# Kernel optimization log

Measured on AMD Instinct MI355X. Metric: run time of the kernel, lower is better.

## Reference

```python
import jax, jax.numpy as jnp
import numpy as np

B, N, F, FOBS, D = 4, 1024, 128, 32, 128
K_HOP = 3  # os.environ k_hop default 3


def setup_inputs() -> dict:
    key = jax.random.key(0)
    k0, k1, k2, k3, k4 = jax.random.split(key, 5)
    X = jax.random.normal(k0, (B, N, F), jnp.float32)
    # xavier-ish scales for params
    a_link = jax.random.normal(k1, (FOBS, 1), jnp.float32) * (1.414 / np.sqrt(FOBS + 1))
    W0 = jax.random.normal(k2, (F, D), jnp.float32) * np.sqrt(2.0 / (F + D))
    W1 = jax.random.normal(k3, (D, D), jnp.float32) * np.sqrt(1.0 / D)
    W2 = jax.random.normal(k4, (D, D), jnp.float32) * np.sqrt(1.0 / D)
    return {"X": X, "a_link": a_link, "W0": W0, "W1": W1, "W2": W2}


def reference(X, a_link, W0, W1, W2):
    eye = jnp.eye(N, dtype=X.dtype)

    def per_graph(Xb):  # Xb: [N, F]
        h = Xb[:, :FOBS]                                   # [N, FOBS]
        # e_ij = a_link^T |h_i - h_j|
        e = jnp.einsum('ijf,fo->ij', jnp.abs(h[:, None, :] - h[None, :, :]), a_link)
        A = jax.nn.sigmoid(e)
        A = A * (1.0 - eye)                                # zero diagonal (A - diag(diag(A)))
        Dm = jnp.zeros_like(A)                             # diag(diag(A)) is zero after removal
        A_hat = A + eye
        d_inv_sqrt = jnp.sum(A_hat, axis=1) ** -0.5        # row sums (dim=1 in mini_batch path)
        norm = d_inv_sqrt[:, None] * A_hat * d_inv_sqrt[None, :]  # D^-1/2 A_hat D^-1/2
        H = norm @ (Xb @ W0)                               # k = 0
        for Wk in (W1, W2):                                # k = 1 .. K_HOP-1 (norm detached in torch)
            H = jax.lax.stop_gradient(norm) @ (H @ Wk)
        return jax.nn.relu(H), A, Dm

    Hs, As, Ds = jax.vmap(per_graph)(X)
    return Hs, As, X, Ds
```

## Files before the change

kernel.cpp:

```cpp
#include <hip/hip_runtime.h>
#include <math.h>

#define BB 4
#define NN 1024
#define FF 128
#define DD 128
#define FOBS 32

typedef __attribute__((ext_vector_type(8))) short bfrag;
typedef __attribute__((ext_vector_type(4))) float ffrag;
typedef __attribute__((ext_vector_type(4))) unsigned short us4;

__device__ __forceinline__ unsigned short f2bf(float x) {
    unsigned u = __builtin_bit_cast(unsigned, x);
    u += 0x7fffu + ((u >> 16) & 1u);
    return (unsigned short)(u >> 16);
}
__device__ __forceinline__ float bf2f(unsigned short s) {
    unsigned u = (unsigned)s << 16;
    return __builtin_bit_cast(float, u);
}
__device__ __forceinline__ void gload16(const void* g, void* l) {
    __builtin_amdgcn_global_load_lds((const __attribute__((address_space(1))) unsigned*)g,
                                     (__attribute__((address_space(3))) unsigned*)l, 16, 0, 0);
}
__device__ __forceinline__ void compute_dinv16(const float* __restrict__ Pp, int b, int n0,
                                               int tid, float* dinv_s) {
    int r = tid >> 4, p = tid & 15;
    float s = Pp[((size_t)b * NN + n0 + r) * 16 + p];
    s += __shfl_xor(s, 1);
    s += __shfl_xor(s, 2);
    s += __shfl_xor(s, 4);
    s += __shfl_xor(s, 8);
    if (p == 0) dinv_s[r] = rsqrtf(1.f + s);
}

__global__ __launch_bounds__(256) void zero_f4(float4* __restrict__ p, int n4) {
    int i = blockIdx.x * 256 + threadIdx.x;
    if (i < n4) p[i] = make_float4(0.f, 0.f, 0.f, 0.f);
}

__global__ __launch_bounds__(256) void adj_kernel(const float* __restrict__ X,
                                                  const float* __restrict__ a_link,
                                                  const float* __restrict__ W0,
                                                  const float* __restrict__ W1,
                                                  const float* __restrict__ W2,
                                                  float* __restrict__ A,
                                                  unsigned short* __restrict__ Abf,
                                                  unsigned short* __restrict__ Xbf,
                                                  unsigned short* __restrict__ Wt,
                                                  float* __restrict__ Pp,
                                                  float* __restrict__ Xo,
                                                  float* __restrict__ Zd) {
    int tid = threadIdx.x;
    if (blockIdx.z == 5) {
        if (Zd) {
            int q = blockIdx.y * 16 + blockIdx.x;
            float4* Z = (float4*)Zd;
#pragma unroll
            for (int p = 0; p < 16; p++)
                Z[(size_t)q * 4096 + p * 256 + tid] = make_float4(0.f, 0.f, 0.f, 0.f);
        }
        return;
    }
    if (blockIdx.z == 4) {
        int q = (blockIdx.y * 16 + blockIdx.x) * 256 + tid;
        if (q < 49152) {
            int m = q >> 14, rem = q & 16383, fp = rem >> 7, f = rem & 127;
            const float* W = (m == 0) ? W0 : (m == 1) ? W1 : W2;
            Wt[q] = f2bf(W[(size_t)f * 128 + fp]);
        } else {
            int u = q - 49152;
#pragma unroll
            for (int p = 0; p < 8; p++) {
                size_t i4 = (size_t)u + (size_t)p * 16384;
                float4 v = *(const float4*)&X[i4 * 4];
                us4 o; o[0] = f2bf(v.x); o[1] = f2bf(v.y); o[2] = f2bf(v.z); o[3] = f2bf(v.w);
                *(us4*)&Xbf[i4 * 4] = o;
            }
        }
        return;
    }
    int b = blockIdx.z, i0 = blockIdx.y * 64, j0 = blockIdx.x * 64;
    __shared__ float hi[64][FOBS + 1];
    __shared__ float hj[64][FOBS + 1];
    __shared__ float av[FOBS];
    __shared__ float part_s[64][16];
    const float* Xb = X + (size_t)b * NN * FF;
    if (j0 == 0) {
#pragma unroll
        for (int p = 0; p < 8; p++) {
            int c = p * 256 + tid, r = c >> 5, qq = c & 31;
            *(float4*)&Xo[((size_t)b * NN + i0 + r) * FF + qq * 4] =
                *(const float4*)&Xb[(size_t)(i0 + r) * FF + qq * 4];
        }
    }
#pragma unroll
    for (int l = 0; l < 8; l++) {
        int idx = l * 256 + tid;
        int r = idx >> 5, f = idx & 31;
        hi[r][f] = Xb[(size_t)(i0 + r) * FF + f];
        hj[r][f] = Xb[(size_t)(j0 + r) * FF + f];
    }
    if (tid < FOBS) av[tid] = a_link[tid];
    __syncthreads();

    int ty = tid >> 4, tx = tid & 15;
    int ir = ty * 4, jc = tx * 4;
    float acc[4][4] = {};
#pragma unroll
    for (int f = 0; f < FOBS; f++) {
        float a = av[f];
        float x[4], y[4];
#pragma unroll
        for (int r = 0; r < 4; r++) x[r] = hi[ir + r][f];
#pragma unroll
        for (int c = 0; c < 4; c++) y[c] = hj[jc + c][f];
#pragma unroll
        for (int r = 0; r < 4; r++)
#pragma unroll
            for (int c = 0; c < 4; c++)
                acc[r][c] += fabsf(x[r] - y[c]) * a;
    }
    float* Ab = A + (size_t)b * NN * NN;
    unsigned short* Abb = Abf + (size_t)b * NN * NN;
#pragma unroll
    for (int r = 0; r < 4; r++) {
        int gi = i0 + ir + r;
        float vv[4];
        float rs = 0.f;
#pragma unroll
        for (int c = 0; c < 4; c++) {
            int gj = j0 + jc + c;
            float sg = 1.f / (1.f + __expf(-acc[r][c]));
            vv[c] = (gi == gj) ? 0.f : sg;
            rs += vv[c];
        }
        *(float4*)&Ab[(size_t)gi * NN + (j0 + jc)] = make_float4(vv[0], vv[1], vv[2], vv[3]);
        us4 o; o[0] = f2bf(vv[0]); o[1] = f2bf(vv[1]); o[2] = f2bf(vv[2]); o[3] = f2bf(vv[3]);
        *(us4*)&Abb[(size_t)gi * NN + (j0 + jc)] = o;
        part_s[ir + r][tx] = rs;
    }
    __syncthreads();
    if (tid < 64) {
        float s = 0.f;
#pragma unroll
        for (int k = 0; k < 16; k++) s += part_s[tid][k];
        Pp[((size_t)b * NN + i0 + tid) * 16 + blockIdx.x] = s;
    }
}

__global__ __launch_bounds__(256) void gw0_kernel(const unsigned short* __restrict__ Xbf,
                                                  const unsigned short* __restrict__ Wt0,
                                                  const float* __restrict__ Pp,
                                                  unsigned short* __restrict__ TtOut) {
    int b = blockIdx.y;
    int n0 = blockIdx.x * 16;
    __shared__ unsigned short Wt_s[128 * 128];
    __shared__ unsigned short H_s[16 * 128];
    __shared__ float dinv_s[16];
    int tid = threadIdx.x;
    compute_dinv16(Pp, b, n0, tid, dinv_s);
    const unsigned short* Hb = Xbf + (size_t)b * NN * DD;
#pragma unroll
    for (int p = 0; p < 8; p++) {
        int c = p * 256 + tid, row = c >> 4, kc = c & 15;
        gload16(Wt0 + (size_t)row * 128 + ((kc ^ (row & 7)) * 8), Wt_s + (size_t)c * 8);
    }
    {
        int c = tid, row = c >> 4, kc = c & 15;
        gload16(Hb + (size_t)(n0 + row) * 128 + ((kc ^ (row & 7)) * 8), H_s + (size_t)c * 8);
    }
    __syncthreads();

    int w = tid >> 6, l = tid & 63, lr = l & 15, lg = l >> 4;
    ffrag acc[2] = {};
#pragma unroll
    for (int ks = 0; ks < 4; ks++) {
        int k0 = ks * 32 + lg * 8;
        bfrag a[2], bb;
#pragma unroll
        for (int rb = 0; rb < 2; rb++) {
            int row = w * 32 + rb * 16 + lr;
            int byt = (row * 256 + k0 * 2) ^ ((row & 7) << 4);
            a[rb] = *(const bfrag*)((const char*)Wt_s + byt);
        }
        {
            int row = lr;
            int byt = (row * 256 + k0 * 2) ^ ((row & 7) << 4);
            bb = *(const bfrag*)((const char*)H_s + byt);
        }
#pragma unroll
        for (int rb = 0; rb < 2; rb++)
            acc[rb] = __builtin_amdgcn_mfma_f32_16x16x32_bf16(a[rb], bb, acc[rb], 0, 0, 0);
    }
    unsigned short* Ttb = TtOut + (size_t)b * DD * NN;
    int nl = lr;
    float dv = dinv_s[nl];
#pragma unroll
    for (int rb = 0; rb < 2; rb++)
#pragma unroll
        for (int r = 0; r < 4; r++) {
            int f = w * 32 + rb * 16 + lg * 4 + r;
            Ttb[(size_t)f * NN + n0 + nl] = f2bf(acc[rb][r] * dv);
        }
}

template <int MODE>
__global__ __launch_bounds__(256) void ga_kernel(const unsigned short* __restrict__ Abf,
                                                 const unsigned short* __restrict__ Tt,
                                                 const unsigned short* __restrict__ WtN,
                                                 const float* __restrict__ Pp,
                                                 unsigned short* __restrict__ TtN,
                                                 float* __restrict__ HsF) {
    int b = blockIdx.y, n0 = blockIdx.x * 16;
    __shared__ unsigned short T_s[3 * 128 * 64];
    __shared__ unsigned short A_s[3 * 16 * 64];
    __shared__ unsigned short W_s[MODE == 0 ? 128 * 128 : 64];
    __shared__ float dinv_s[16];
    int tid = threadIdx.x;
    const unsigned short* Ttb = Tt + (size_t)b * DD * NN;
    const unsigned short* Ab = Abf + (size_t)b * NN * NN;

    compute_dinv16(Pp, b, n0, tid, dinv_s);

    if (MODE == 0) {
#pragma unroll
        for (int p = 0; p < 8; p++) {
            int c = p * 256 + tid, row = c >> 4, kc = c & 15;
            gload16(WtN + (size_t)row * 128 + ((kc ^ (row & 7)) * 8), W_s + (size_t)c * 8);
        }
    }
    auto stageT = [&](int buf, int kt) {
#pragma unroll
        for (int p = 0; p < 4; p++) {
            int c = p * 256 + tid, row = c >> 3, kc = c & 7;
            gload16(Ttb + (size_t)row * NN + kt + ((kc ^ (row & 7)) * 8),
                    T_s + (size_t)buf * (128 * 64) + (size_t)c * 8);
        }
        int c = tid & 127, row = c >> 3, kc = c & 7;
        gload16(Ab + (size_t)(n0 + row) * NN + kt + ((kc ^ (row & 7)) * 8),
                A_s + (size_t)buf * (16 * 64) + (size_t)c * 8);
    };
    stageT(0, 0);
    stageT(1, 64);

    int w = tid >> 6, l = tid & 63, lr = l & 15, lg = l >> 4;
    ffrag acc[2] = {};
    int cur = 0, sb = 2;
    for (int t = 0; t < 16; t++) {
        if (t <= 13) stageT(sb, (t + 2) * 64);
        if (t < 14)       asm volatile("s_waitcnt vmcnt(10)" ::: "memory");
        else if (t == 14) asm volatile("s_waitcnt vmcnt(5)"  ::: "memory");
        else              asm volatile("s_waitcnt vmcnt(0)"  ::: "memory");
        __builtin_amdgcn_s_barrier();
        asm volatile("" ::: "memory");
        const unsigned short* Tc = T_s + (size_t)cur * (128 * 64);
        const unsigned short* Ac = A_s + (size_t)cur * (16 * 64);
#pragma unroll
        for (int ks = 0; ks < 2; ks++) {
            int k0 = ks * 32 + lg * 8;
            bfrag a[2], bb;
#pragma unroll
            for (int rb = 0; rb < 2; rb++) {
                int row = w * 32 + rb * 16 + lr;
                int byt = (row * 128 + k0 * 2) ^ ((row & 7) << 4);
                a[rb] = *(const bfrag*)((const char*)Tc + byt);
            }
            {
                int row = lr;
                int byt = (row * 128 + k0 * 2) ^ ((row & 7) << 4);
                bb = *(const bfrag*)((const char*)Ac + byt);
            }
#pragma unroll
            for (int rb = 0; rb < 2; rb++)
                acc[rb] = __builtin_amdgcn_mfma_f32_16x16x32_bf16(a[rb], bb, acc[rb], 0, 0, 0);
        }
        asm volatile("s_waitcnt lgkmcnt(0)" ::: "memory");
        __builtin_amdgcn_s_barrier();
        cur = (cur == 2) ? 0 : cur + 1;
        sb = (sb == 2) ? 0 : sb + 1;
    }

    int nl = lr;
    float dv = dinv_s[nl];
    if (MODE == 1) {
#pragma unroll
        for (int rb = 0; rb < 2; rb++) {
            int f0 = w * 32 + rb * 16 + lg * 4;
            float v[4];
#pragma unroll
            for (int r = 0; r < 4; r++) {
                float idv = bf2f(Ttb[(size_t)(f0 + r) * NN + n0 + nl]);
                v[r] = fmaxf((acc[rb][r] + idv) * dv, 0.f);
            }
            *(float4*)&HsF[((size_t)b * NN + n0 + nl) * DD + f0] = make_float4(v[0], v[1], v[2], v[3]);
        }
        return;
    }
    unsigned short* H_s = T_s;
#pragma unroll
    for (int rb = 0; rb < 2; rb++) {
        int f0 = w * 32 + rb * 16 + lg * 4;
        us4 o;
#pragma unroll
        for (int r = 0; r < 4; r++) {
            float idv = bf2f(Ttb[(size_t)(f0 + r) * NN + n0 + nl]);
            o[r] = f2bf((acc[rb][r] + idv) * dv);
        }
        int byt = (nl * 256 + f0 * 2) ^ ((nl & 7) << 4);
        *(us4*)((char*)H_s + byt) = o;
    }
    __syncthreads();
    ffrag acc2[2] = {};
#pragma unroll
    for (int ks = 0; ks < 4; ks++) {
        int k0 = ks * 32 + lg * 8;
        bfrag a2[2], b2;
#pragma unroll
        for (int rb = 0; rb < 2; rb++) {
            int row = w * 32 + rb * 16 + lr;
            int byt = (row * 256 + k0 * 2) ^ ((row & 7) << 4);
            a2[rb] = *(const bfrag*)((const char*)W_s + byt);
        }
        {
            int row = lr;
            int byt = (row * 256 + k0 * 2) ^ ((row & 7) << 4);
            b2 = *(const bfrag*)((const char*)H_s + byt);
        }
#pragma unroll
        for (int rb = 0; rb < 2; rb++)
            acc2[rb] = __builtin_amdgcn_mfma_f32_16x16x32_bf16(a2[rb], b2, acc2[rb], 0, 0, 0);
    }
    unsigned short* TtNb = TtN + (size_t)b * DD * NN;
#pragma unroll
    for (int rb = 0; rb < 2; rb++)
#pragma unroll
        for (int r = 0; r < 4; r++) {
            int f2 = w * 32 + rb * 16 + lg * 4 + r;
            TtNb[(size_t)f2 * NN + n0 + nl] = f2bf(acc2[rb][r] * dv);
        }
}

extern "C" void kernel_launch(void* const* d_in, const int* in_sizes, int n_in,
                              void* d_out, int out_size, void* d_ws, size_t ws_size,
                              hipStream_t stream) {
    const float* X      = (const float*)d_in[0];
    const float* a_link = (const float*)d_in[1];
    const float* W0     = (const float*)d_in[2];
    const float* W1     = (const float*)d_in[3];
    const float* W2     = (const float*)d_in[4];
    float* out = (float*)d_out;

    const size_t HND = (size_t)BB * NN * DD;
    const size_t HNN = (size_t)BB * NN * NN;
    float* Hs = out;
    float* As = out + HND;
    float* Xo = out + HND + HNN;
    float* Ds = out + 2 * HND + HNN;

    const size_t NEED = 11894784;
    bool usews = (ws_size >= NEED);
    char* scr = usews ? (char*)d_ws : (char*)Ds;

    unsigned short* Abf = (unsigned short*)(scr);
    unsigned short* Xbf = (unsigned short*)(scr + 8388608);
    unsigned short* TtA = (unsigned short*)(scr + 9437184);
    unsigned short* TtB = (unsigned short*)(scr + 10485760);
    unsigned short* Wt  = (unsigned short*)(scr + 11534336);
    float* Pp           = (float*)(scr + 11632640);

    adj_kernel<<<dim3(16, 16, usews ? 6 : 5), 256, 0, stream>>>(
        X, a_link, W0, W1, W2, As, Abf, Xbf, Wt, Pp, Xo, usews ? Ds : nullptr);

    gw0_kernel<<<dim3(64, BB), 256, 0, stream>>>(Xbf, Wt, Pp, TtA);
    ga_kernel<0><<<dim3(64, BB), 256, 0, stream>>>(Abf, TtA, Wt + 16384, Pp, TtB, nullptr);
    ga_kernel<0><<<dim3(64, BB), 256, 0, stream>>>(Abf, TtB, Wt + 32768, Pp, TtA, nullptr);
    ga_kernel<1><<<dim3(64, BB), 256, 0, stream>>>(Abf, TtA, nullptr, Pp, nullptr, Hs);

    if (!usews)
        zero_f4<<<dim3(4096), 256, 0, stream>>>((float4*)Ds, (int)(HNN / 4));
}
```

Measured before the change: 48.70 us.

## Fuse all stages into one persistent kernel with grid barriers and folded normalization

```diff
diff --git a/kernel.cpp b/kernel.cpp
--- a/kernel.cpp
+++ b/kernel.cpp
@@ -6,6 +6,7 @@
 #define FF 128
 #define DD 128
 #define FOBS 32
+#define NBLK 256
 
 typedef __attribute__((ext_vector_type(8))) short bfrag;
 typedef __attribute__((ext_vector_type(4))) float ffrag;
@@ -16,231 +17,40 @@
     u += 0x7fffu + ((u >> 16) & 1u);
     return (unsigned short)(u >> 16);
 }
-__device__ __forceinline__ float bf2f(unsigned short s) {
-    unsigned u = (unsigned)s << 16;
-    return __builtin_bit_cast(float, u);
-}
 __device__ __forceinline__ void gload16(const void* g, void* l) {
     __builtin_amdgcn_global_load_lds((const __attribute__((address_space(1))) unsigned*)g,
                                      (__attribute__((address_space(3))) unsigned*)l, 16, 0, 0);
 }
-__device__ __forceinline__ void compute_dinv16(const float* __restrict__ Pp, int b, int n0,
-                                               int tid, float* dinv_s) {
-    int r = tid >> 4, p = tid & 15;
-    float s = Pp[((size_t)b * NN + n0 + r) * 16 + p];
-    s += __shfl_xor(s, 1);
-    s += __shfl_xor(s, 2);
-    s += __shfl_xor(s, 4);
-    s += __shfl_xor(s, 8);
-    if (p == 0) dinv_s[r] = rsqrtf(1.f + s);
-}
-
-__global__ __launch_bounds__(256) void zero_f4(float4* __restrict__ p, int n4) {
-    int i = blockIdx.x * 256 + threadIdx.x;
-    if (i < n4) p[i] = make_float4(0.f, 0.f, 0.f, 0.f);
-}
-
-__global__ __launch_bounds__(256) void adj_kernel(const float* __restrict__ X,
-                                                  const float* __restrict__ a_link,
-                                                  const float* __restrict__ W0,
-                                                  const float* __restrict__ W1,
-                                                  const float* __restrict__ W2,
-                                                  float* __restrict__ A,
-                                                  unsigned short* __restrict__ Abf,
-                                                  unsigned short* __restrict__ Xbf,
-                                                  unsigned short* __restrict__ Wt,
-                                                  float* __restrict__ Pp,
-                                                  float* __restrict__ Xo,
-                                                  float* __restrict__ Zd) {
-    int tid = threadIdx.x;
-    if (blockIdx.z == 5) {
-        if (Zd) {
-            int q = blockIdx.y * 16 + blockIdx.x;
-            float4* Z = (float4*)Zd;
-#pragma unroll
-            for (int p = 0; p < 16; p++)
-                Z[(size_t)q * 4096 + p * 256 + tid] = make_float4(0.f, 0.f, 0.f, 0.f);
-        }
-        return;
-    }
-    if (blockIdx.z == 4) {
-        int q = (blockIdx.y * 16 + blockIdx.x) * 256 + tid;
-        if (q < 49152) {
-            int m = q >> 14, rem = q & 16383, fp = rem >> 7, f = rem & 127;
-            const float* W = (m == 0) ? W0 : (m == 1) ? W1 : W2;
-            Wt[q] = f2bf(W[(size_t)f * 128 + fp]);
-        } else {
-            int u = q - 49152;
-#pragma unroll
-            for (int p = 0; p < 8; p++) {
-                size_t i4 = (size_t)u + (size_t)p * 16384;
-                float4 v = *(const float4*)&X[i4 * 4];
-                us4 o; o[0] = f2bf(v.x); o[1] = f2bf(v.y); o[2] = f2bf(v.z); o[3] = f2bf(v.w);
-                *(us4*)&Xbf[i4 * 4] = o;
-            }
-        }
-        return;
-    }
-    int b = blockIdx.z, i0 = blockIdx.y * 64, j0 = blockIdx.x * 64;
-    __shared__ float hi[64][FOBS + 1];
-    __shared__ float hj[64][FOBS + 1];
-    __shared__ float av[FOBS];
-    __shared__ float part_s[64][16];
-    const float* Xb = X + (size_t)b * NN * FF;
-    if (j0 == 0) {
-#pragma unroll
-        for (int p = 0; p < 8; p++) {
-            int c = p * 256 + tid, r = c >> 5, qq = c & 31;
-            *(float4*)&Xo[((size_t)b * NN + i0 + r) * FF + qq * 4] =
-                *(const float4*)&Xb[(size_t)(i0 + r) * FF + qq * 4];
-        }
-    }
-#pragma unroll
-    for (int l = 0; l < 8; l++) {
-        int idx = l * 256 + tid;
-        int r = idx >> 5, f = idx & 31;
-        hi[r][f] = Xb[(size_t)(i0 + r) * FF + f];
-        hj[r][f] = Xb[(size_t)(j0 + r) * FF + f];
-    }
-    if (tid < FOBS) av[tid] = a_link[tid];
+__device__ __forceinline__ void gbar(unsigned* cnt) {
     __syncthreads();
-
-    int ty = tid >> 4, tx = tid & 15;
-    int ir = ty * 4, jc = tx * 4;
-    float acc[4][4] = {};
-#pragma unroll
-    for (int f = 0; f < FOBS; f++) {
-        float a = av[f];
-        float x[4], y[4];
-#pragma unroll
-        for (int r = 0; r < 4; r++) x[r] = hi[ir + r][f];
-#pragma unroll
-        for (int c = 0; c < 4; c++) y[c] = hj[jc + c][f];
-#pragma unroll
-        for (int r = 0; r < 4; r++)
-#pragma unroll
-            for (int c = 0; c < 4; c++)
-                acc[r][c] += fabsf(x[r] - y[c]) * a;
-    }
-    float* Ab = A + (size_t)b * NN * NN;
-    unsigned short* Abb = Abf + (size_t)b * NN * NN;
-#pragma unroll
-    for (int r = 0; r < 4; r++) {
-        int gi = i0 + ir + r;
-        float vv[4];
-        float rs = 0.f;
-#pragma unroll
-        for (int c = 0; c < 4; c++) {
-            int gj = j0 + jc + c;
-            float sg = 1.f / (1.f + __expf(-acc[r][c]));
-            vv[c] = (gi == gj) ? 0.f : sg;
-            rs += vv[c];
-        }
-        *(float4*)&Ab[(size_t)gi * NN + (j0 + jc)] = make_float4(vv[0], vv[1], vv[2], vv[3]);
-        us4 o; o[0] = f2bf(vv[0]); o[1] = f2bf(vv[1]); o[2] = f2bf(vv[2]); o[3] = f2bf(vv[3]);
-        *(us4*)&Abb[(size_t)gi * NN + (j0 + jc)] = o;
-        part_s[ir + r][tx] = rs;
+    if (threadIdx.x == 0) {
+        __threadfence();
+        __hip_atomic_fetch_add(cnt, 1u, __ATOMIC_RELAXED, __HIP_MEMORY_SCOPE_AGENT);
+        while (__hip_atomic_load(cnt, __ATOMIC_RELAXED, __HIP_MEMORY_SCOPE_AGENT) < NBLK)
+            __builtin_amdgcn_s_sleep(8);
+        __threadfence();
     }
     __syncthreads();
-    if (tid < 64) {
-        float s = 0.f;
-#pragma unroll
-        for (int k = 0; k < 16; k++) s += part_s[tid][k];
-        Pp[((size_t)b * NN + i0 + tid) * 16 + blockIdx.x] = s;
-    }
-}
-
-__global__ __launch_bounds__(256) void gw0_kernel(const unsigned short* __restrict__ Xbf,
-                                                  const unsigned short* __restrict__ Wt0,
-                                                  const float* __restrict__ Pp,
-                                                  unsigned short* __restrict__ TtOut) {
-    int b = blockIdx.y;
-    int n0 = blockIdx.x * 16;
-    __shared__ unsigned short Wt_s[128 * 128];
-    __shared__ unsigned short H_s[16 * 128];
-    __shared__ float dinv_s[16];
-    int tid = threadIdx.x;
-    compute_dinv16(Pp, b, n0, tid, dinv_s);
-    const unsigned short* Hb = Xbf + (size_t)b * NN * DD;
-#pragma unroll
-    for (int p = 0; p < 8; p++) {
-        int c = p * 256 + tid, row = c >> 4, kc = c & 15;
-        gload16(Wt0 + (size_t)row * 128 + ((kc ^ (row & 7)) * 8), Wt_s + (size_t)c * 8);
-    }
-    {
-        int c = tid, row = c >> 4, kc = c & 15;
-        gload16(Hb + (size_t)(n0 + row) * 128 + ((kc ^ (row & 7)) * 8), H_s + (size_t)c * 8);
-    }
-    __syncthreads();
-
-    int w = tid >> 6, l = tid & 63, lr = l & 15, lg = l >> 4;
-    ffrag acc[2] = {};
-#pragma unroll
-    for (int ks = 0; ks < 4; ks++) {
-        int k0 = ks * 32 + lg * 8;
-        bfrag a[2], bb;
-#pragma unroll
-        for (int rb = 0; rb < 2; rb++) {
-            int row = w * 32 + rb * 16 + lr;
-            int byt = (row * 256 + k0 * 2) ^ ((row & 7) << 4);
-            a[rb] = *(const bfrag*)((const char*)Wt_s + byt);
-        }
-        {
-            int row = lr;
-            int byt = (row * 256 + k0 * 2) ^ ((row & 7) << 4);
-            bb = *(const bfrag*)((const char*)H_s + byt);
-        }
-#pragma unroll
-        for (int rb = 0; rb < 2; rb++)
-            acc[rb] = __builtin_amdgcn_mfma_f32_16x16x32_bf16(a[rb], bb, acc[rb], 0, 0, 0);
-    }
-    unsigned short* Ttb = TtOut + (size_t)b * DD * NN;
-    int nl = lr;
-    float dv = dinv_s[nl];
-#pragma unroll
-    for (int rb = 0; rb < 2; rb++)
-#pragma unroll
-        for (int r = 0; r < 4; r++) {
-            int f = w * 32 + rb * 16 + lg * 4 + r;
-            Ttb[(size_t)f * NN + n0 + nl] = f2bf(acc[rb][r] * dv);
-        }
-}
-
-template <int MODE>
-__global__ __launch_bounds__(256) void ga_kernel(const unsigned short* __restrict__ Abf,
-                                                 const unsigned short* __restrict__ Tt,
-                                                 const unsigned short* __restrict__ WtN,
-                                                 const float* __restrict__ Pp,
-                                                 unsigned short* __restrict__ TtN,
-                                                 float* __restrict__ HsF) {
-    int b = blockIdx.y, n0 = blockIdx.x * 16;
-    __shared__ unsigned short T_s[3 * 128 * 64];
-    __shared__ unsigned short A_s[3 * 16 * 64];
-    __shared__ unsigned short W_s[MODE == 0 ? 128 * 128 : 64];
-    __shared__ float dinv_s[16];
-    int tid = threadIdx.x;
-    const unsigned short* Ttb = Tt + (size_t)b * DD * NN;
-    const unsigned short* Ab = Abf + (size_t)b * NN * NN;
-
-    compute_dinv16(Pp, b, n0, tid, dinv_s);
-
-    if (MODE == 0) {
-#pragma unroll
-        for (int p = 0; p < 8; p++) {
-            int c = p * 256 + tid, row = c >> 4, kc = c & 15;
-            gload16(WtN + (size_t)row * 128 + ((kc ^ (row & 7)) * 8), W_s + (size_t)c * 8);
-        }
-    }
+}
+
+template <int LAST>
+__device__ __forceinline__ void ga_phase(const unsigned short* __restrict__ Sb,
+                                         const unsigned short* __restrict__ Tin,
+                                         unsigned short* __restrict__ Tout,
+                                         float* __restrict__ HsB,
+                                         int n0, int tid, char* smem) {
+    unsigned short* T_s = (unsigned short*)smem;
+    unsigned short* S_s = (unsigned short*)(smem + 49152);
     auto stageT = [&](int buf, int kt) {
 #pragma unroll
         for (int p = 0; p < 4; p++) {
             int c = p * 256 + tid, row = c >> 3, kc = c & 7;
-            gload16(Ttb + (size_t)row * NN + kt + ((kc ^ (row & 7)) * 8),
+            gload16(Tin + (size_t)row * NN + kt + ((kc ^ (row & 7)) * 8),
                     T_s + (size_t)buf * (128 * 64) + (size_t)c * 8);
         }
         int c = tid & 127, row = c >> 3, kc = c & 7;
-        gload16(Ab + (size_t)(n0 + row) * NN + kt + ((kc ^ (row & 7)) * 8),
-                A_s + (size_t)buf * (16 * 64) + (size_t)c * 8);
+        gload16(Sb + (size_t)(n0 + row) * NN + kt + ((kc ^ (row & 7)) * 8),
+                S_s + (size_t)buf * (16 * 64) + (size_t)c * 8);
     };
     stageT(0, 0);
     stageT(1, 64);
@@ -256,7 +66,7 @@
         __builtin_amdgcn_s_barrier();
         asm volatile("" ::: "memory");
         const unsigned short* Tc = T_s + (size_t)cur * (128 * 64);
-        const unsigned short* Ac = A_s + (size_t)cur * (16 * 64);
+        const unsigned short* Sc = S_s + (size_t)cur * (16 * 64);
 #pragma unroll
         for (int ks = 0; ks < 2; ks++) {
             int k0 = ks * 32 + lg * 8;
@@ -270,7 +80,7 @@
             {
                 int row = lr;
                 int byt = (row * 128 + k0 * 2) ^ ((row & 7) << 4);
-                bb = *(const bfrag*)((const char*)Ac + byt);
+                bb = *(const bfrag*)((const char*)Sc + byt);
             }
 #pragma unroll
             for (int rb = 0; rb < 2; rb++)
@@ -281,65 +91,268 @@
         cur = (cur == 2) ? 0 : cur + 1;
         sb = (sb == 2) ? 0 : sb + 1;
     }
-
-    int nl = lr;
-    float dv = dinv_s[nl];
-    if (MODE == 1) {
+    if (LAST) {
 #pragma unroll
         for (int rb = 0; rb < 2; rb++) {
             int f0 = w * 32 + rb * 16 + lg * 4;
             float v[4];
 #pragma unroll
+            for (int r = 0; r < 4; r++) v[r] = fmaxf(acc[rb][r], 0.f);
+            *(float4*)&HsB[(size_t)(n0 + lr) * DD + f0] = make_float4(v[0], v[1], v[2], v[3]);
+        }
+    } else {
+#pragma unroll
+        for (int rb = 0; rb < 2; rb++)
+#pragma unroll
             for (int r = 0; r < 4; r++) {
-                float idv = bf2f(Ttb[(size_t)(f0 + r) * NN + n0 + nl]);
-                v[r] = fmaxf((acc[rb][r] + idv) * dv, 0.f);
-            }
-            *(float4*)&HsF[((size_t)b * NN + n0 + nl) * DD + f0] = make_float4(v[0], v[1], v[2], v[3]);
-        }
-        return;
-    }
-    unsigned short* H_s = T_s;
-#pragma unroll
-    for (int rb = 0; rb < 2; rb++) {
-        int f0 = w * 32 + rb * 16 + lg * 4;
-        us4 o;
-#pragma unroll
-        for (int r = 0; r < 4; r++) {
-            float idv = bf2f(Ttb[(size_t)(f0 + r) * NN + n0 + nl]);
-            o[r] = f2bf((acc[rb][r] + idv) * dv);
-        }
-        int byt = (nl * 256 + f0 * 2) ^ ((nl & 7) << 4);
-        *(us4*)((char*)H_s + byt) = o;
-    }
-    __syncthreads();
-    ffrag acc2[2] = {};
-#pragma unroll
-    for (int ks = 0; ks < 4; ks++) {
-        int k0 = ks * 32 + lg * 8;
-        bfrag a2[2], b2;
+                int f = w * 32 + rb * 16 + lg * 4 + r;
+                Tout[(size_t)f * NN + n0 + lr] = f2bf(acc[rb][r]);
+            }
+    }
+}
+
+__global__ __launch_bounds__(256, 1) void fused_kernel(
+    const float* __restrict__ X, const float* __restrict__ a_link,
+    const float* __restrict__ W0, const float* __restrict__ W1, const float* __restrict__ W2,
+    float* __restrict__ As, float* __restrict__ Xo, float* __restrict__ Hs,
+    float* __restrict__ Ds,
+    unsigned short* __restrict__ Sbf, unsigned short* __restrict__ Xbf,
+    unsigned short* __restrict__ TtX, unsigned short* __restrict__ TtY,
+    unsigned short* __restrict__ W01t, unsigned short* __restrict__ W2t,
+    float* __restrict__ Pp, unsigned* cnt, int usews)
+{
+    __shared__ __align__(16) char smem[77824];
+    int tid = threadIdx.x;
+    int bid = blockIdx.x;
+
+    {
+        float* hi   = (float*)smem;
+        float* hj   = (float*)(smem + 8448);
+        float* av   = (float*)(smem + 16896);
+        float* part = (float*)(smem + 17024);
+        if (tid < FOBS) av[tid] = a_link[tid];
+        for (int it = 0; it < 4; it++) {
+            int t = bid * 4 + it;
+            int bt = t >> 8, rem = t & 255;
+            int i0 = (rem >> 4) * 64, j0 = (rem & 15) * 64;
+            const float* Xb = X + (size_t)bt * NN * FF;
+            __syncthreads();
+            if (j0 == 0) {
+#pragma unroll
+                for (int p = 0; p < 8; p++) {
+                    int c = p * 256 + tid, r = c >> 5, qq = c & 31;
+                    *(float4*)&Xo[((size_t)bt * NN + i0 + r) * FF + qq * 4] =
+                        *(const float4*)&Xb[(size_t)(i0 + r) * FF + qq * 4];
+                }
+            }
+#pragma unroll
+            for (int lq = 0; lq < 8; lq++) {
+                int idx = lq * 256 + tid;
+                int r = idx >> 5, f = idx & 31;
+                hi[r * 33 + f] = Xb[(size_t)(i0 + r) * FF + f];
+                hj[r * 33 + f] = Xb[(size_t)(j0 + r) * FF + f];
+            }
+            __syncthreads();
+            int ty = tid >> 4, tx = tid & 15;
+            int ir = ty * 4, jc = tx * 4;
+            float acc[4][4] = {};
+#pragma unroll
+            for (int f = 0; f < FOBS; f++) {
+                float a = av[f];
+                float x[4], y[4];
+#pragma unroll
+                for (int r = 0; r < 4; r++) x[r] = hi[(ir + r) * 33 + f];
+#pragma unroll
+                for (int c = 0; c < 4; c++) y[c] = hj[(jc + c) * 33 + f];
+#pragma unroll
+                for (int r = 0; r < 4; r++)
+#pragma unroll
+                    for (int c = 0; c < 4; c++)
+                        acc[r][c] += fabsf(x[r] - y[c]) * a;
+            }
+            float* Ab = As + (size_t)bt * NN * NN;
+#pragma unroll
+            for (int r = 0; r < 4; r++) {
+                int gi = i0 + ir + r;
+                float vv[4]; float rs = 0.f;
+#pragma unroll
+                for (int c = 0; c < 4; c++) {
+                    int gj = j0 + jc + c;
+                    float sg = 1.f / (1.f + __expf(-acc[r][c]));
+                    vv[c] = (gi == gj) ? 0.f : sg;
+                    rs += vv[c];
+                }
+                *(float4*)&Ab[(size_t)gi * NN + (j0 + jc)] = make_float4(vv[0], vv[1], vv[2], vv[3]);
+                part[(ir + r) * 16 + tx] = rs;
+            }
+            __syncthreads();
+            if (tid < 64) {
+                float s = 0.f;
+#pragma unroll
+                for (int k = 0; k < 16; k++) s += part[tid * 16 + k];
+                Pp[((size_t)bt * NN + i0 + tid) * 16 + (rem & 15)] = s;
+            }
+        }
+        if (bid < 16) {
+#pragma unroll
+            for (int q = 0; q < 4; q++) {
+                int e = q * 256 + tid;
+                int g = bid * 8 + (e >> 7), f = e & 127;
+                float s = 0.f;
+                for (int h = 0; h < 128; h++) s += W0[f * 128 + h] * W1[h * 128 + g];
+                W01t[g * 128 + f] = f2bf(s);
+            }
+        } else if (bid < 32) {
+#pragma unroll
+            for (int q = 0; q < 4; q++) {
+                int e = (bid - 16) * 1024 + q * 256 + tid;
+                int f2 = e >> 7, g = e & 127;
+                W2t[e] = f2bf(W2[g * 128 + f2]);
+            }
+        } else if (bid < 96) {
+#pragma unroll
+            for (int q = 0; q < 8; q++) {
+                size_t i4 = (size_t)(bid - 32) * 2048 + q * 256 + tid;
+                float4 v = *(const float4*)&X[i4 * 4];
+                us4 o; o[0] = f2bf(v.x); o[1] = f2bf(v.y); o[2] = f2bf(v.z); o[3] = f2bf(v.w);
+                *(us4*)&Xbf[i4 * 4] = o;
+            }
+        }
+    }
+    gbar(cnt + 0);
+
+    int b = bid >> 6, n0 = (bid & 63) * 16;
+    {
+        float* dinvF         = (float*)smem;
+        unsigned short* W01s = (unsigned short*)(smem + 4096);
+        unsigned short* W2s  = (unsigned short*)(smem + 36864);
+        unsigned short* Xps  = (unsigned short*)(smem + 69632);
+        unsigned short* Ps   = (unsigned short*)(smem + 73728);
+        const unsigned short* Xb = Xbf + (size_t)b * NN * DD;
+#pragma unroll
+        for (int p = 0; p < 8; p++) {
+            int c = p * 256 + tid, row = c >> 4, kc = c & 15;
+            gload16(W01t + (size_t)row * 128 + ((kc ^ (row & 7)) * 8), W01s + (size_t)c * 8);
+        }
+#pragma unroll
+        for (int p = 0; p < 8; p++) {
+            int c = p * 256 + tid, row = c >> 4, kc = c & 15;
+            gload16(W2t + (size_t)row * 128 + ((kc ^ (row & 7)) * 8), W2s + (size_t)c * 8);
+        }
+        {
+            int c = tid, row = c >> 4, kc = c & 15;
+            gload16(Xb + (size_t)(n0 + row) * 128 + ((kc ^ (row & 7)) * 8), Xps + (size_t)c * 8);
+        }
+#pragma unroll
+        for (int rr = 0; rr < 4; rr++) {
+            int row = tid * 4 + rr;
+            const float* pp = Pp + ((size_t)b * NN + row) * 16;
+            float s = 0.f;
+#pragma unroll
+            for (int k2 = 0; k2 < 16; k2++) s += pp[k2];
+            dinvF[row] = rsqrtf(1.f + s);
+        }
+        __syncthreads();
+        {
+            int r = tid >> 4, cg = tid & 15;
+            int gi = n0 + r;
+            const float* Ar = As + ((size_t)b * NN + gi) * NN;
+            unsigned short* Sr = Sbf + ((size_t)b * NN + gi) * NN;
+            float di = dinvF[gi];
+#pragma unroll
+            for (int c4 = 0; c4 < 16; c4++) {
+                int col = cg * 4 + c4 * 64;
+                float4 a4 = *(const float4*)&Ar[col];
+                us4 o;
+                o[0] = f2bf(di * dinvF[col + 0] * (a4.x + ((col + 0) == gi ? 1.f : 0.f)));
+                o[1] = f2bf(di * dinvF[col + 1] * (a4.y + ((col + 1) == gi ? 1.f : 0.f)));
+                o[2] = f2bf(di * dinvF[col + 2] * (a4.z + ((col + 2) == gi ? 1.f : 0.f)));
+                o[3] = f2bf(di * dinvF[col + 3] * (a4.w + ((col + 3) == gi ? 1.f : 0.f)));
+                *(us4*)&Sr[col] = o;
+            }
+        }
+        if (usews) {
+            float4* Z = (float4*)Ds;
+#pragma unroll
+            for (int q = 0; q < 16; q++)
+                Z[(size_t)bid * 4096 + q * 256 + tid] = make_float4(0.f, 0.f, 0.f, 0.f);
+        }
+        int w = tid >> 6, l = tid & 63, lr = l & 15, lg = l >> 4;
+        ffrag pacc[2] = {};
+#pragma unroll
+        for (int ks = 0; ks < 4; ks++) {
+            int k0 = ks * 32 + lg * 8;
+            bfrag a[2], bb;
+#pragma unroll
+            for (int rb = 0; rb < 2; rb++) {
+                int row = w * 32 + rb * 16 + lr;
+                int byt = (row * 256 + k0 * 2) ^ ((row & 7) << 4);
+                a[rb] = *(const bfrag*)((const char*)W01s + byt);
+            }
+            {
+                int byt = (lr * 256 + k0 * 2) ^ ((lr & 7) << 4);
+                bb = *(const bfrag*)((const char*)Xps + byt);
+            }
+#pragma unroll
+            for (int rb = 0; rb < 2; rb++)
+                pacc[rb] = __builtin_amdgcn_mfma_f32_16x16x32_bf16(a[rb], bb, pacc[rb], 0, 0, 0);
+        }
 #pragma unroll
         for (int rb = 0; rb < 2; rb++) {
-            int row = w * 32 + rb * 16 + lr;
-            int byt = (row * 256 + k0 * 2) ^ ((row & 7) << 4);
-            a2[rb] = *(const bfrag*)((const char*)W_s + byt);
-        }
-        {
-            int row = lr;
-            int byt = (row * 256 + k0 * 2) ^ ((row & 7) << 4);
-            b2 = *(const bfrag*)((const char*)H_s + byt);
-        }
+            int g0 = w * 32 + rb * 16 + lg * 4;
+            us4 o;
+#pragma unroll
+            for (int r = 0; r < 4; r++) o[r] = f2bf(pacc[rb][r]);
+            int byt = (lr * 256 + g0 * 2) ^ ((lr & 7) << 4);
+            *(us4*)((char*)Ps + byt) = o;
+        }
+        __syncthreads();
+        ffrag tacc[2] = {};
+#pragma unroll
+        for (int ks = 0; ks < 4; ks++) {
+            int k0 = ks * 32 + lg * 8;
+            bfrag a2[2], b2;
+#pragma unroll
+            for (int rb = 0; rb < 2; rb++) {
+                int row = w * 32 + rb * 16 + lr;
+                int byt = (row * 256 + k0 * 2) ^ ((row & 7) << 4);
+                a2[rb] = *(const bfrag*)((const char*)W2s + byt);
+            }
+            {
+                int byt = (lr * 256 + k0 * 2) ^ ((lr & 7) << 4);
+                b2 = *(const bfrag*)((const char*)Ps + byt);
+            }
+#pragma unroll
+            for (int rb = 0; rb < 2; rb++)
+                tacc[rb] = __builtin_amdgcn_mfma_f32_16x16x32_bf16(a2[rb], b2, tacc[rb], 0, 0, 0);
+        }
+        unsigned short* Tb = TtX + (size_t)b * DD * NN;
 #pragma unroll
         for (int rb = 0; rb < 2; rb++)
-            acc2[rb] = __builtin_amdgcn_mfma_f32_16x16x32_bf16(a2[rb], b2, acc2[rb], 0, 0, 0);
-    }
-    unsigned short* TtNb = TtN + (size_t)b * DD * NN;
-#pragma unroll
-    for (int rb = 0; rb < 2; rb++)
-#pragma unroll
-        for (int r = 0; r < 4; r++) {
-            int f2 = w * 32 + rb * 16 + lg * 4 + r;
-            TtNb[(size_t)f2 * NN + n0 + nl] = f2bf(acc2[rb][r] * dv);
-        }
+#pragma unroll
+            for (int r = 0; r < 4; r++) {
+                int f2 = w * 32 + rb * 16 + lg * 4 + r;
+                Tb[(size_t)f2 * NN + n0 + lr] = f2bf(tacc[rb][r]);
+            }
+    }
+    gbar(cnt + 1);
+
+    const unsigned short* Sb = Sbf + (size_t)b * NN * NN;
+    unsigned short* TXb = TtX + (size_t)b * DD * NN;
+    unsigned short* TYb = TtY + (size_t)b * DD * NN;
+    ga_phase<0>(Sb, TXb, TYb, nullptr, n0, tid, smem);
+    gbar(cnt + 2);
+    ga_phase<0>(Sb, TYb, TXb, nullptr, n0, tid, smem);
+    gbar(cnt + 3);
+    ga_phase<1>(Sb, TXb, nullptr, Hs + (size_t)b * NN * DD, n0, tid, smem);
+
+    if (!usews) {
+        gbar(cnt + 4);
+        float4* Z = (float4*)Ds;
+#pragma unroll
+        for (int q = 0; q < 16; q++)
+            Z[(size_t)bid * 4096 + q * 256 + tid] = make_float4(0.f, 0.f, 0.f, 0.f);
+    }
 }
 
 extern "C" void kernel_launch(void* const* d_in, const int* in_sizes, int n_in,
@@ -359,25 +372,21 @@
     float* Xo = out + HND + HNN;
     float* Ds = out + 2 * HND + HNN;
 
-    const size_t NEED = 11894784;
+    const size_t NEED = 11862080;
     bool usews = (ws_size >= NEED);
     char* scr = usews ? (char*)d_ws : (char*)Ds;
 
-    unsigned short* Abf = (unsigned short*)(scr);
-    unsigned short* Xbf = (unsigned short*)(scr + 8388608);
-    unsigned short* TtA = (unsigned short*)(scr + 9437184);
-    unsigned short* TtB = (unsigned short*)(scr + 10485760);
-    unsigned short* Wt  = (unsigned short*)(scr + 11534336);
-    float* Pp           = (float*)(scr + 11632640);
-
-    adj_kernel<<<dim3(16, 16, usews ? 6 : 5), 256, 0, stream>>>(
-        X, a_link, W0, W1, W2, As, Abf, Xbf, Wt, Pp, Xo, usews ? Ds : nullptr);
-
-    gw0_kernel<<<dim3(64, BB), 256, 0, stream>>>(Xbf, Wt, Pp, TtA);
-    ga_kernel<0><<<dim3(64, BB), 256, 0, stream>>>(Abf, TtA, Wt + 16384, Pp, TtB, nullptr);
-    ga_kernel<0><<<dim3(64, BB), 256, 0, stream>>>(Abf, TtB, Wt + 32768, Pp, TtA, nullptr);
-    ga_kernel<1><<<dim3(64, BB), 256, 0, stream>>>(Abf, TtA, nullptr, Pp, nullptr, Hs);
-
-    if (!usews)
-        zero_f4<<<dim3(4096), 256, 0, stream>>>((float4*)Ds, (int)(HNN / 4));
-}
+    unsigned short* Sbf  = (unsigned short*)(scr);
+    unsigned short* Xbf  = (unsigned short*)(scr + 8388608);
+    unsigned short* TtX  = (unsigned short*)(scr + 9437184);
+    unsigned short* TtY  = (unsigned short*)(scr + 10485760);
+    unsigned short* W01t = (unsigned short*)(scr + 11534336);
+    unsigned short* W2t  = (unsigned short*)(scr + 11567104);
+    float* Pp            = (float*)(scr + 11599872);
+    unsigned* cnt        = (unsigned*)(scr + 11862016);
+
+    hipMemsetAsync(cnt, 0, 64, stream);
+    fused_kernel<<<dim3(NBLK), dim3(256), 0, stream>>>(
+        X, a_link, W0, W1, W2, As, Xo, Hs, Ds,
+        Sbf, Xbf, TtX, TtY, W01t, W2t, Pp, cnt, usews ? 1 : 0);
+}
```

Result: slower. 156.2 us (+220.7%).
